# Kernel optimization log

Hardware: AMD Instinct MI355X
Metric: run time of the kernel (lower is better)

## Reference

```python
import jax, jax.numpy as jnp
import numpy as np

N = 512            # feature grid rows
M = 512            # feature grid cols
FEAT = 100         # FEATURE_SIZE
FREQ = 16          # frequencies
NPTS = 1048576     # number of UV query points
FFIN = FEAT + 2 * (2 * FREQ + 1)  # 166
DIMS = [FFIN, 128, 128, 128, 128, 3]


def setup_inputs() -> dict:
    key = jax.random.key(0)
    ks = jax.random.split(key, 2 + 2 * 5)
    inp = {
        "UV": jax.random.uniform(ks[0], (NPTS, 2), dtype=jnp.float32),
        "features": jax.random.uniform(ks[1], (N, M, FEAT), dtype=jnp.float32),
    }
    # 5-layer MLP params (torch nn.Linear-style uniform init)
    for i in range(5):
        fan_in = DIMS[i]
        bound = 1.0 / np.sqrt(fan_in)
        inp[f"W{i}"] = jax.random.uniform(ks[2 + 2 * i], (DIMS[i], DIMS[i + 1]),
                                          dtype=jnp.float32, minval=-bound, maxval=bound)
        inp[f"b{i}"] = jax.random.uniform(ks[3 + 2 * i], (DIMS[i + 1],),
                                          dtype=jnp.float32, minval=-bound, maxval=bound)
    return inp


def _posenc(UV):
    # torch order: [UV, sin(1*UV), cos(1*UV), sin(2*UV), cos(2*UV), ...]
    X = [UV]
    for i in range(FREQ):
        k = float(2 ** i)
        X.append(jnp.sin(k * UV))
        X.append(jnp.cos(k * UV))
    return jnp.concatenate(X, axis=-1)  # [..., 2*(2*FREQ+1)]


def reference(UV, features, W0, b0, W1, b1, W2, b2, W3, b3, W4, b4):
    U, V = UV[..., 0], UV[..., 1]
    iU = (N - 1) * U
    iV = (M - 1) * V
    iU0 = jnp.floor(iU).astype(jnp.int32)
    iU1 = jnp.ceil(iU).astype(jnp.int32)
    iV0 = jnp.floor(iV).astype(jnp.int32)
    iV1 = jnp.ceil(iV).astype(jnp.int32)
    fu = (iU - iU0)[..., None]  # fractional weights, [NPTS,1]
    fv = (iV - iV0)[..., None]
    # bilinear gather of 100-dim features (4 irregular gathers)
    feat = (features[iU0, iV0] * (1.0 - fu) * (1.0 - fv)
            + features[iU1, iV0] * fu * (1.0 - fv)
            + features[iU0, iV1] * (1.0 - fu) * fv
            + features[iU1, iV1] * fu * fv)
    x = jnp.concatenate([_posenc(UV), feat], axis=-1)  # [NPTS, 166]
    lrelu = lambda z: jax.nn.leaky_relu(z, negative_slope=0.01)
    h = lrelu(x @ W0 + b0)
    h = lrelu(h @ W1 + b1)
    h = lrelu(h @ W2 + b2)
    h = lrelu(h @ W3 + b3)
    return h @ W4 + b4  # [NPTS, 3]
```

## Files before the change

### kernel.cpp

```cpp
#include <hip/hip_runtime.h>


#define GN    512
#define TP    64
#define STR0  184
#define STR1  136

#define WOFF1 22528
#define WOFF2 38912
#define WOFF3 55296
#define W4OFF 71680

typedef _Float16 half8  __attribute__((ext_vector_type(8)));
typedef _Float16 half4v __attribute__((ext_vector_type(4)));
typedef float    f4     __attribute__((ext_vector_type(4)));
typedef float    f16v   __attribute__((ext_vector_type(16)));


__global__ __launch_bounds__(256) void k_prep(
    const float* __restrict__ W0, const float* __restrict__ W1,
    const float* __restrict__ W2, const float* __restrict__ W3,
    const float* __restrict__ W4, _Float16* __restrict__ wt,
    const float* __restrict__ UV, int* __restrict__ hist) {
  int b = blockIdx.x;
  if (b < 282) {
    int t = b * 256 + threadIdx.x;
    if (t >= 72064) return;
    float v;
    if (t < 22528) {
      int j = t & 7, l = (t >> 3) & 63, g = t >> 9;
      int ks = g % 11;
      int ot = g / 11;
      int k = 16 * ks + 8 * (l >> 5) + j;
      int n = ot * 32 + (l & 31);
      if (k < 100)      v = W0[(66 + k) * 128 + n];
      else if (k < 166) v = W0[(k - 100) * 128 + n];
      else              v = 0.0f;
    } else if (t < 71680) {
      int u = t - 22528;
      int layer = u >> 14, r = u & 16383;
      int j = r & 7, l = (r >> 3) & 63, ks = (r >> 9) & 7, ot = r >> 12;
      int k = 16 * ks + 8 * (l >> 5) + j;
      int n = ot * 32 + (l & 31);
      const float* W = (layer == 0) ? W1 : (layer == 1) ? W2 : W3;
      v = W[k * 128 + n];
    } else {
      int u2 = t - 71680;
      int qt = u2 / 96, r = u2 - 96 * qt;
      int kk = r / 3, e = r - 3 * kk;
      v = W4[(qt * 32 + kk) * 3 + e];
    }
    wt[t] = (_Float16)v;
  } else if (hist != nullptr) {
    int i = (b - 282) * 256 + threadIdx.x;
    float2 uv = ((const float2*)UV)[i];
    int iU0 = (int)floorf(511.0f * uv.x);
    int iV0 = (int)floorf(511.0f * uv.y);
    atomicAdd(&hist[iU0 * 32 + (iV0 >> 4)], 1);
  }
}

__device__ __forceinline__ int point_bin(float U, float V) {
  int iU0 = (int)floorf(511.0f * U);
  int iV0 = (int)floorf(511.0f * V);
  return iU0 * 32 + (iV0 >> 4);
}

__global__ __launch_bounds__(256) void k_scanA(const int* __restrict__ hist,
                                               int* __restrict__ binoff,
                                               int* __restrict__ bsum) {
  __shared__ int s[256];
  int t = threadIdx.x, g = blockIdx.x * 256 + t;
  int v = hist[g];
  s[t] = v;
  __syncthreads();
  for (int d = 1; d < 256; d <<= 1) {
    int x = (t >= d) ? s[t - d] : 0;
    __syncthreads();
    s[t] += x;
    __syncthreads();
  }
  binoff[g] = s[t] - v;
  if (t == 255) bsum[blockIdx.x] = s[t];
}

__global__ __launch_bounds__(64) void k_scanB(const int* __restrict__ bsum,
                                              int* __restrict__ bbase) {
  __shared__ int s[64];
  int t = threadIdx.x;
  int v = bsum[t];
  s[t] = v;
  __syncthreads();
  for (int d = 1; d < 64; d <<= 1) {
    int x = (t >= d) ? s[t - d] : 0;
    __syncthreads();
    s[t] += x;
    __syncthreads();
  }
  bbase[t] = s[t] - v;
}

__global__ __launch_bounds__(256) void k_scatter(const float* __restrict__ UV,
                                                 int* __restrict__ binoff,
                                                 const int* __restrict__ bbase,
                                                 float4* __restrict__ sorted) {
  int i = blockIdx.x * 256 + threadIdx.x;
  float2 uv = ((const float2*)UV)[i];
  int bin = point_bin(uv.x, uv.y);
  int pos = atomicAdd(&binoff[bin], 1) + bbase[bin >> 8];
  sorted[pos] = make_float4(uv.x, uv.y, __int_as_float(i), 0.0f);
}

__device__ __forceinline__ half8 ld8h(const float* __restrict__ p, bool full) {
  f4 lo = *(const f4*)p;
  f4 hi;
  if (full) hi = *(const f4*)(p + 4);
  else      { hi[0] = 0.f; hi[1] = 0.f; hi[2] = 0.f; hi[3] = 0.f; }
  half8 h;
  h[0] = (_Float16)lo[0]; h[1] = (_Float16)lo[1];
  h[2] = (_Float16)lo[2]; h[3] = (_Float16)lo[3];
  h[4] = (_Float16)hi[0]; h[5] = (_Float16)hi[1];
  h[6] = (_Float16)hi[2]; h[7] = (_Float16)hi[3];
  return h;
}

template <bool PF>
__device__ __forceinline__ void layerPF(const half8 (&A)[8], half8 (&An)[8],
    const _Float16* __restrict__ wfn,
    const _Float16* Gin, _Float16* Gout, const float* __restrict__ bp,
    int lane, int nl, int kh, int ot) {
  f4 bf[4];
#pragma unroll
  for (int g = 0; g < 4; ++g)
    bf[g] = *(const f4*)(bp + ot * 32 + 4 * kh + 8 * g);
  f16v a0, a1;
#pragma unroll
  for (int r = 0; r < 16; ++r) { a0[r] = 0.f; a1[r] = 0.f; }
#pragma unroll
  for (int ks = 0; ks < 4; ++ks) {
    half8 B0 = *(const half8*)(Gin + nl * STR1 + ks * 16 + kh * 8);
    half8 B1 = *(const half8*)(Gin + (32 + nl) * STR1 + ks * 16 + kh * 8);
    a0 = __builtin_amdgcn_mfma_f32_32x32x16_f16(A[ks], B0, a0, 0, 0, 0);
    a1 = __builtin_amdgcn_mfma_f32_32x32x16_f16(A[ks], B1, a1, 0, 0, 0);
  }
  if constexpr (PF) {
#pragma unroll
    for (int k2 = 0; k2 < 8; ++k2)
      An[k2] = *(const half8*)(wfn + ((ot * 8 + k2) * 64 + lane) * 8);
  }
#pragma unroll
  for (int ks = 4; ks < 8; ++ks) {
    half8 B0 = *(const half8*)(Gin + nl * STR1 + ks * 16 + kh * 8);
    half8 B1 = *(const half8*)(Gin + (32 + nl) * STR1 + ks * 16 + kh * 8);
    a0 = __builtin_amdgcn_mfma_f32_32x32x16_f16(A[ks], B0, a0, 0, 0, 0);
    a1 = __builtin_amdgcn_mfma_f32_32x32x16_f16(A[ks], B1, a1, 0, 0, 0);
  }
#pragma unroll
  for (int g = 0; g < 4; ++g) {
    half4v h0, h1;
#pragma unroll
    for (int i = 0; i < 4; ++i) {
      float z0 = a0[4 * g + i] + bf[g][i]; z0 = fmaxf(z0, 0.01f * z0);
      float z1 = a1[4 * g + i] + bf[g][i]; z1 = fmaxf(z1, 0.01f * z1);
      h0[i] = (_Float16)z0; h1[i] = (_Float16)z1;
    }
    int col = ot * 32 + 4 * kh + 8 * g;
    *(half4v*)(Gout + nl * STR1 + col) = h0;
    *(half4v*)(Gout + (32 + nl) * STR1 + col) = h1;
  }
}

template <int MODE>
__global__ __launch_bounds__(256, 4) void k_main(
    const float* __restrict__ UV, const float4* __restrict__ sorted,
    const _Float16* __restrict__ wt, const float* __restrict__ F,
    const float* __restrict__ b0, const float* __restrict__ b1,
    const float* __restrict__ b2, const float* __restrict__ b3,
    const float* __restrict__ b4, float* __restrict__ out) {
  __shared__ _Float16 bufA[TP * STR0] __attribute__((aligned(16)));
  __shared__ _Float16 bufB[TP * STR1] __attribute__((aligned(16)));
  const int t = threadIdx.x;
  const int lane = t & 63;
  const int nl = lane & 31;
  const int kh = lane >> 5;
  const int ot = t >> 6;
  const int pFE = t >> 2;
  const int sFE = t & 3;

  half8 A0[11];
#pragma unroll
  for (int ks = 0; ks < 11; ++ks)
    A0[ks] = *(const half8*)(wt + ((ot * 11 + ks) * 64 + lane) * 8);
  half8 A1[8], A2[8], A3[8];

  float U, V;
  int oidx;
  if constexpr (MODE == 2) {
    float4 s4 = sorted[blockIdx.x * TP + pFE];
    U = s4.x; V = s4.y; oidx = __float_as_int(s4.z);
  } else {
    oidx = blockIdx.x * TP + pFE;
    float2 uv = ((const float2*)UV)[oidx];
    U = uv.x; V = uv.y;
  }

  if (sFE == 0) {
    bufA[pFE * STR0 + 100] = (_Float16)U;
    bufA[pFE * STR0 + 101] = (_Float16)V;
  }
  if (sFE == 1) {
#pragma unroll
    for (int c = 166; c < 176; ++c) bufA[pFE * STR0 + c] = (_Float16)0.0f;
  }
  if (sFE == 2) *(int*)&bufB[pFE * STR1 + 128] = oidx;

  {
    const float inv2pi = 0.15915494309189535f;
    float Ur = U * inv2pi, Vr = V * inv2pi;
#pragma unroll
    for (int fi = 0; fi < 4; ++fi) {
      int f = 4 * fi + sFE;
      float kk = (float)(1 << f);
      float ru = kk * Ur; ru -= floorf(ru);
      float rv = kk * Vr; rv -= floorf(rv);
      float su = __builtin_amdgcn_sinf(ru);
      float cu = __builtin_amdgcn_cosf(ru);
      float sv = __builtin_amdgcn_sinf(rv);
      float cv = __builtin_amdgcn_cosf(rv);
      int cbase = pFE * STR0 + 102 + 4 * f;
      bufA[cbase + 0] = (_Float16)su;
      bufA[cbase + 1] = (_Float16)sv;
      bufA[cbase + 2] = (_Float16)cu;
      bufA[cbase + 3] = (_Float16)cv;
    }
  }

  {
    float iu = 511.0f * U, iv = 511.0f * V;
    float fu0 = floorf(iu), fv0 = floorf(iv);
    int iU0 = (int)fu0, iV0 = (int)fv0;
    int iU1 = (int)ceilf(iu), iV1 = (int)ceilf(iv);
    float fu = iu - fu0, fv = iv - fv0;
    float w00 = (1.f - fu) * (1.f - fv);
    float w10 = fu * (1.f - fv);
    float w01 = (1.f - fu) * fv;
    float w11 = fu * fv;
    const float* F00 = F + (size_t)(iU0 * GN + iV0) * 100;
    const float* F01 = F + (size_t)(iU0 * GN + iV1) * 100;
    const float* F10 = F + (size_t)(iU1 * GN + iV0) * 100;
    const float* F11 = F + (size_t)(iU1 * GN + iV1) * 100;
    _Float16 h00 = (_Float16)w00, h01 = (_Float16)w01;
    _Float16 h10 = (_Float16)w10, h11 = (_Float16)w11;
    half8 v00, v01, v10, v11;
#pragma unroll
    for (int e = 0; e < 8; ++e) { v00[e]=h00; v01[e]=h01; v10[e]=h10; v11[e]=h11; }
    for (int j = sFE; j < 13; j += 4) {
      bool full = (j < 12);
      half8 a = ld8h(F00 + 8 * j, full);
      half8 b = ld8h(F01 + 8 * j, full);
      half8 c = ld8h(F10 + 8 * j, full);
      half8 d = ld8h(F11 + 8 * j, full);
      half8 o = a * v00 + b * v01 + c * v10 + d * v11;
      if (full) {
        *(half8*)&bufA[pFE * STR0 + 8 * j] = o;
      } else {
        half4v o4; o4[0]=o[0]; o4[1]=o[1]; o4[2]=o[2]; o4[3]=o[3];
        *(half4v*)&bufA[pFE * STR0 + 96] = o4;
      }
    }
  }
  __syncthreads();

  {
    f4 bf[4];
#pragma unroll
    for (int g = 0; g < 4; ++g)
      bf[g] = *(const f4*)(b0 + ot * 32 + 4 * kh + 8 * g);
    f16v a0, a1;
#pragma unroll
    for (int r = 0; r < 16; ++r) { a0[r] = 0.f; a1[r] = 0.f; }
#pragma unroll
    for (int ks = 0; ks < 8; ++ks) {
      half8 B0 = *(const half8*)&bufA[nl * STR0 + ks * 16 + kh * 8];
      half8 B1 = *(const half8*)&bufA[(32 + nl) * STR0 + ks * 16 + kh * 8];
      a0 = __builtin_amdgcn_mfma_f32_32x32x16_f16(A0[ks], B0, a0, 0, 0, 0);
      a1 = __builtin_amdgcn_mfma_f32_32x32x16_f16(A0[ks], B1, a1, 0, 0, 0);
    }
#pragma unroll
    for (int k2 = 0; k2 < 8; ++k2)
      A1[k2] = *(const half8*)(wt + WOFF1 + ((ot * 8 + k2) * 64 + lane) * 8);
#pragma unroll
    for (int ks = 8; ks < 11; ++ks) {
      half8 B0 = *(const half8*)&bufA[nl * STR0 + ks * 16 + kh * 8];
      half8 B1 = *(const half8*)&bufA[(32 + nl) * STR0 + ks * 16 + kh * 8];
      a0 = __builtin_amdgcn_mfma_f32_32x32x16_f16(A0[ks], B0, a0, 0, 0, 0);
      a1 = __builtin_amdgcn_mfma_f32_32x32x16_f16(A0[ks], B1, a1, 0, 0, 0);
    }
#pragma unroll
    for (int g = 0; g < 4; ++g) {
      half4v h0, h1;
#pragma unroll
      for (int i = 0; i < 4; ++i) {
        float z0 = a0[4 * g + i] + bf[g][i]; z0 = fmaxf(z0, 0.01f * z0);
        float z1 = a1[4 * g + i] + bf[g][i]; z1 = fmaxf(z1, 0.01f * z1);
        h0[i] = (_Float16)z0; h1[i] = (_Float16)z1;
      }
      int col = ot * 32 + 4 * kh + 8 * g;
      *(half4v*)&bufB[nl * STR1 + col] = h0;
      *(half4v*)&bufB[(32 + nl) * STR1 + col] = h1;
    }
  }
  __syncthreads();
  layerPF<true >(A1, A2, wt + WOFF2, bufB, bufA, b1, lane, nl, kh, ot);
  __syncthreads();
  layerPF<true >(A2, A3, wt + WOFF3, bufA, bufB, b2, lane, nl, kh, ot);
  __syncthreads();
  layerPF<false>(A3, A3, wt,         bufB, bufA, b3, lane, nl, kh, ot);
  __syncthreads();

  {
    int pp = t >> 2, qt = t & 3;
    const _Float16* h4 = &bufA[pp * STR1 + qt * 32];
    const _Float16* w4 = wt + W4OFF + qt * 96;
    float y0 = 0.f, y1 = 0.f, y2 = 0.f;
#pragma unroll
    for (int c = 0; c < 4; ++c) {
      half8 hv = *(const half8*)(h4 + 8 * c);
      half8 wa = *(const half8*)(w4 + c * 24);
      half8 wb = *(const half8*)(w4 + c * 24 + 8);
      half8 wc = *(const half8*)(w4 + c * 24 + 16);
      _Float16 wf[24];
      *(half8*)&wf[0] = wa; *(half8*)&wf[8] = wb; *(half8*)&wf[16] = wc;
#pragma unroll
      for (int e8 = 0; e8 < 8; ++e8) {
        float vf = (float)hv[e8];
        y0 += vf * (float)wf[e8 * 3 + 0];
        y1 += vf * (float)wf[e8 * 3 + 1];
        y2 += vf * (float)wf[e8 * 3 + 2];
      }
    }
    y0 += __shfl_xor(y0, 1); y0 += __shfl_xor(y0, 2);
    y1 += __shfl_xor(y1, 1); y1 += __shfl_xor(y1, 2);
    y2 += __shfl_xor(y2, 1); y2 += __shfl_xor(y2, 2);
    if (qt == 0) {
      int op;
      if constexpr (MODE == 2) op = *(const int*)&bufB[pp * STR1 + 128];
      else                     op = blockIdx.x * TP + pp;
      out[(size_t)op * 3 + 0] = y0 + b4[0];
      out[(size_t)op * 3 + 1] = y1 + b4[1];
      out[(size_t)op * 3 + 2] = y2 + b4[2];
    }
  }
}

extern "C" void kernel_launch(void* const* d_in, const int* in_sizes, int n_in,
                              void* d_out, int out_size, void* d_ws, size_t ws_size,
                              hipStream_t stream) {
  const float* UV  = (const float*)d_in[0];
  const float* FEA = (const float*)d_in[1];
  const float* W0  = (const float*)d_in[2];
  const float* b0  = (const float*)d_in[3];
  const float* W1  = (const float*)d_in[4];
  const float* b1  = (const float*)d_in[5];
  const float* W2  = (const float*)d_in[6];
  const float* b2  = (const float*)d_in[7];
  const float* W3  = (const float*)d_in[8];
  const float* b3  = (const float*)d_in[9];
  const float* W4  = (const float*)d_in[10];
  const float* b4  = (const float*)d_in[11];
  float* out = (float*)d_out;

  char* ws = (char*)d_ws;
  _Float16* wt = (_Float16*)ws;
  int*    hist   = (int*)(ws + 147456);
  int*    binoff = (int*)(ws + 212992);
  int*    bsum   = (int*)(ws + 278528);
  int*    bbase  = (int*)(ws + 278784);
  float4* sorted = (float4*)(ws + 294912);

  const size_t needSort = 294912ull + 16777216ull;

  const int nblk = 1048576 / TP;

  if (ws_size >= needSort) {
    hipMemsetAsync(hist, 0, 65536, stream);
    k_prep<<<282 + 4096, 256, 0, stream>>>(W0, W1, W2, W3, W4, wt, UV, hist);
    k_scanA<<<64, 256, 0, stream>>>(hist, binoff, bsum);
    k_scanB<<<1, 64, 0, stream>>>(bsum, bbase);
    k_scatter<<<4096, 256, 0, stream>>>(UV, binoff, bbase, sorted);
    k_main<2><<<nblk, 256, 0, stream>>>(UV, sorted, wt, FEA,
                                        b0, b1, b2, b3, b4, out);
  } else {
    k_prep<<<282, 256, 0, stream>>>(W0, W1, W2, W3, W4, wt, UV, nullptr);
    k_main<1><<<nblk, 256, 0, stream>>>(UV, nullptr, wt, FEA,
                                        b0, b1, b2, b3, b4, out);
  }
}
```

Baseline: 495.2 us.

## Run MLP layers in place in one LDS buffer and raise occupancy hint

Drops the second shared-memory activation buffer. Each layer now reads and writes a single buffer, with an extra barrier between the MFMA reads and the writeback. It keeps the output index in a register instead of LDS and raises the launch-bounds min-blocks hint from 4 to 6. Together these aim to let more workgroups reside per CU, at the cost of one more barrier per layer and tighter register limits that could cause spills.

```diff
diff --git a/kernel.cpp b/kernel.cpp
--- a/kernel.cpp
+++ b/kernel.cpp
@@ -4,7 +4,6 @@
 #define GN    512
 #define TP    64
 #define STR0  184
-#define STR1  136
 
 #define WOFF1 22528
 #define WOFF2 38912
@@ -125,9 +124,9 @@
 }
 
 template <bool PF>
-__device__ __forceinline__ void layerPF(const half8 (&A)[8], half8 (&An)[8],
+__device__ __forceinline__ void layerIP(const half8 (&A)[8], half8 (&An)[8],
     const _Float16* __restrict__ wfn,
-    const _Float16* Gin, _Float16* Gout, const float* __restrict__ bp,
+    _Float16* G, const float* __restrict__ bp,
     int lane, int nl, int kh, int ot) {
   f4 bf[4];
 #pragma unroll
@@ -138,8 +137,8 @@
   for (int r = 0; r < 16; ++r) { a0[r] = 0.f; a1[r] = 0.f; }
 #pragma unroll
   for (int ks = 0; ks < 4; ++ks) {
-    half8 B0 = *(const half8*)(Gin + nl * STR1 + ks * 16 + kh * 8);
-    half8 B1 = *(const half8*)(Gin + (32 + nl) * STR1 + ks * 16 + kh * 8);
+    half8 B0 = *(const half8*)(G + nl * STR0 + ks * 16 + kh * 8);
+    half8 B1 = *(const half8*)(G + (32 + nl) * STR0 + ks * 16 + kh * 8);
     a0 = __builtin_amdgcn_mfma_f32_32x32x16_f16(A[ks], B0, a0, 0, 0, 0);
     a1 = __builtin_amdgcn_mfma_f32_32x32x16_f16(A[ks], B1, a1, 0, 0, 0);
   }
@@ -150,11 +149,12 @@
   }
 #pragma unroll
   for (int ks = 4; ks < 8; ++ks) {
-    half8 B0 = *(const half8*)(Gin + nl * STR1 + ks * 16 + kh * 8);
-    half8 B1 = *(const half8*)(Gin + (32 + nl) * STR1 + ks * 16 + kh * 8);
+    half8 B0 = *(const half8*)(G + nl * STR0 + ks * 16 + kh * 8);
+    half8 B1 = *(const half8*)(G + (32 + nl) * STR0 + ks * 16 + kh * 8);
     a0 = __builtin_amdgcn_mfma_f32_32x32x16_f16(A[ks], B0, a0, 0, 0, 0);
     a1 = __builtin_amdgcn_mfma_f32_32x32x16_f16(A[ks], B1, a1, 0, 0, 0);
   }
+  __syncthreads();
 #pragma unroll
   for (int g = 0; g < 4; ++g) {
     half4v h0, h1;
@@ -165,20 +165,19 @@
       h0[i] = (_Float16)z0; h1[i] = (_Float16)z1;
     }
     int col = ot * 32 + 4 * kh + 8 * g;
-    *(half4v*)(Gout + nl * STR1 + col) = h0;
-    *(half4v*)(Gout + (32 + nl) * STR1 + col) = h1;
+    *(half4v*)(G + nl * STR0 + col) = h0;
+    *(half4v*)(G + (32 + nl) * STR0 + col) = h1;
   }
 }
 
 template <int MODE>
-__global__ __launch_bounds__(256, 4) void k_main(
+__global__ __launch_bounds__(256, 6) void k_main(
     const float* __restrict__ UV, const float4* __restrict__ sorted,
     const _Float16* __restrict__ wt, const float* __restrict__ F,
     const float* __restrict__ b0, const float* __restrict__ b1,
     const float* __restrict__ b2, const float* __restrict__ b3,
     const float* __restrict__ b4, float* __restrict__ out) {
   __shared__ _Float16 bufA[TP * STR0] __attribute__((aligned(16)));
-  __shared__ _Float16 bufB[TP * STR1] __attribute__((aligned(16)));
   const int t = threadIdx.x;
   const int lane = t & 63;
   const int nl = lane & 31;
@@ -212,7 +211,6 @@
 #pragma unroll
     for (int c = 166; c < 176; ++c) bufA[pFE * STR0 + c] = (_Float16)0.0f;
   }
-  if (sFE == 2) *(int*)&bufB[pFE * STR1 + 128] = oidx;
 
   {
     const float inv2pi = 0.15915494309189535f;
@@ -296,6 +294,7 @@
       a0 = __builtin_amdgcn_mfma_f32_32x32x16_f16(A0[ks], B0, a0, 0, 0, 0);
       a1 = __builtin_amdgcn_mfma_f32_32x32x16_f16(A0[ks], B1, a1, 0, 0, 0);
     }
+    __syncthreads();
 #pragma unroll
     for (int g = 0; g < 4; ++g) {
       half4v h0, h1;
@@ -306,22 +305,21 @@
         h0[i] = (_Float16)z0; h1[i] = (_Float16)z1;
       }
       int col = ot * 32 + 4 * kh + 8 * g;
-      *(half4v*)&bufB[nl * STR1 + col] = h0;
-      *(half4v*)&bufB[(32 + nl) * STR1 + col] = h1;
-    }
-  }
-  __syncthreads();
-  layerPF<true >(A1, A2, wt + WOFF2, bufB, bufA, b1, lane, nl, kh, ot);
-  __syncthreads();
-  layerPF<true >(A2, A3, wt + WOFF3, bufA, bufB, b2, lane, nl, kh, ot);
-  __syncthreads();
-  layerPF<false>(A3, A3, wt,         bufB, bufA, b3, lane, nl, kh, ot);
+      *(half4v*)&bufA[nl * STR0 + col] = h0;
+      *(half4v*)&bufA[(32 + nl) * STR0 + col] = h1;
+    }
+  }
+  __syncthreads();
+  layerIP<true >(A1, A2, wt + WOFF2, bufA, b1, lane, nl, kh, ot);
+  __syncthreads();
+  layerIP<true >(A2, A3, wt + WOFF3, bufA, b2, lane, nl, kh, ot);
+  __syncthreads();
+  layerIP<false>(A3, A3, wt,         bufA, b3, lane, nl, kh, ot);
   __syncthreads();
 
   {
-    int pp = t >> 2, qt = t & 3;
-    const _Float16* h4 = &bufA[pp * STR1 + qt * 32];
-    const _Float16* w4 = wt + W4OFF + qt * 96;
+    const _Float16* h4 = &bufA[pFE * STR0 + sFE * 32];
+    const _Float16* w4 = wt + W4OFF + sFE * 96;
     float y0 = 0.f, y1 = 0.f, y2 = 0.f;
 #pragma unroll
     for (int c = 0; c < 4; ++c) {
@@ -342,13 +340,10 @@
     y0 += __shfl_xor(y0, 1); y0 += __shfl_xor(y0, 2);
     y1 += __shfl_xor(y1, 1); y1 += __shfl_xor(y1, 2);
     y2 += __shfl_xor(y2, 1); y2 += __shfl_xor(y2, 2);
-    if (qt == 0) {
-      int op;
-      if constexpr (MODE == 2) op = *(const int*)&bufB[pp * STR1 + 128];
-      else                     op = blockIdx.x * TP + pp;
-      out[(size_t)op * 3 + 0] = y0 + b4[0];
-      out[(size_t)op * 3 + 1] = y1 + b4[1];
-      out[(size_t)op * 3 + 2] = y2 + b4[2];
+    if (sFE == 0) {
+      out[(size_t)oidx * 3 + 0] = y0 + b4[0];
+      out[(size_t)oidx * 3 + 1] = y1 + b4[1];
+      out[(size_t)oidx * 3 + 2] = y2 + b4[2];
     }
   }
 }
```

Result: slower. 672.9 us (+35.9%).
